# Kernel optimization log

Hardware: AMD Instinct MI355X
Metric: run time of the kernel (lower is better)

The kernel has to match this reference:

```python
import jax, jax.numpy as jnp
import numpy as np

B, S, D_IN, D_OUT, E, K = 4, 2048, 1024, 1024, 8, 2


def setup_inputs() -> dict:
    key = jax.random.key(0)
    ks = jax.random.split(key, 6)
    scale_in = 1.0 / np.sqrt(D_IN)
    return {
        "x": jax.random.normal(ks[0], (B, S, D_IN), dtype=jnp.float32),
        "gate_w": jax.random.uniform(ks[1], (E, D_IN), jnp.float32, -scale_in, scale_in),
        "gate_b": jax.random.uniform(ks[2], (E,), jnp.float32, -scale_in, scale_in),
        "expert_biases": jnp.zeros((E,), dtype=jnp.float32),
        "expert_w": jax.random.uniform(ks[3], (E, D_OUT, D_IN), jnp.float32, -scale_in, scale_in),
        "expert_b": jax.random.uniform(ks[4], (E, D_OUT), jnp.float32, -scale_in, scale_in),
    }


def reference(x, gate_w, gate_b, expert_biases, expert_w, expert_b):
    # Gating: sigmoid(Linear(x) + expert_biases), then top-k over experts
    gate_logits = jnp.einsum("bsd,ed->bse", x, gate_w) + gate_b + expert_biases
    gate_probs = jax.nn.sigmoid(gate_logits)
    top_k_probs, top_k_indices = jax.lax.top_k(gate_probs, K)  # [B,S,K]
    top_k_probs = top_k_probs / jnp.sum(top_k_probs, axis=-1, keepdims=True)

    # Dense all-expert compute: stack[e,b,s,o]
    expert_outputs = jnp.einsum("bsd,eod->ebso", x, expert_w) + expert_b[:, None, None, :]

    # Faithful reproduction of the original gather/permute:
    # result[b,s,j,o] = expert_outputs[tki[b,s,j], b, s, j]  (feature index is j, not o)
    bi = jnp.arange(B)[:, None, None]
    si = jnp.arange(S)[None, :, None]
    ji = jnp.arange(K)[None, None, :]
    val = expert_outputs[top_k_indices, bi, si, ji]  # [B,S,K]

    weighted = jnp.sum(val * top_k_probs, axis=-1)  # [B,S]
    final_output = jnp.broadcast_to(weighted[..., None], (B, S, D_OUT))
    return final_output, top_k_indices
```

## Files before the change

### kernel.cpp

```cpp
#include <hip/hip_runtime.h>
#include <math.h>

#define TOKENS 8192
#define DIN    1024
#define DOUT   1024
#define NE     8

typedef float vf4 __attribute__((ext_vector_type(4)));

__global__ __launch_bounds__(512, 4) void moe_fused(
    const float* __restrict__ x,
    const float* __restrict__ gate_w,
    const float* __restrict__ gate_b,
    const float* __restrict__ expert_biases,
    const float* __restrict__ expert_w,
    const float* __restrict__ expert_b,
    float* __restrict__ out,
    float* __restrict__ out_idx) {
  __shared__ float lgate[NE * DIN];

  {
    const vf4* src = (const vf4*)gate_w;
    vf4* dst = (vf4*)lgate;
#pragma unroll
    for (int i = 0; i < 4; ++i)
      dst[threadIdx.x + 512 * i] = src[threadIdx.x + 512 * i];
  }

  const int t    = blockIdx.x * 8 + (threadIdx.x >> 6);
  const int lane = threadIdx.x & 63;

  vf4 xa[4];
  const vf4* xr = (const vf4*)(x + (size_t)t * DIN);
#pragma unroll
  for (int i = 0; i < 4; ++i) xa[i] = xr[lane + 64 * i];

  __syncthreads();

  float za[NE];
#pragma unroll
  for (int e = 0; e < NE; ++e) za[e] = 0.f;
#pragma unroll
  for (int i = 0; i < 4; ++i) {
    vf4 w[NE];
#pragma unroll
    for (int e = 0; e < NE; ++e)
      w[e] = ((const vf4*)(lgate + e * DIN))[lane + 64 * i];
#pragma unroll
    for (int e = 0; e < NE; ++e)
      za[e] += xa[i].x * w[e].x + xa[i].y * w[e].y + xa[i].z * w[e].z + xa[i].w * w[e].w;
  }

#pragma unroll
  for (int off = 32; off > 0; off >>= 1) {
    float tmp[NE];
#pragma unroll
    for (int e = 0; e < NE; ++e) tmp[e] = __shfl_xor(za[e], off, 64);
#pragma unroll
    for (int e = 0; e < NE; ++e) za[e] += tmp[e];
  }
#pragma unroll
  for (int e = 0; e < NE; ++e) za[e] += gate_b[e] + expert_biases[e];

  int e0 = 0; float z0 = za[0];
#pragma unroll
  for (int e = 1; e < NE; ++e) if (za[e] > z0) { z0 = za[e]; e0 = e; }
  int e1 = (e0 == 0) ? 1 : 0; float z1 = za[e1];
#pragma unroll
  for (int e = 0; e < NE; ++e) if (e != e0 && za[e] > z1) { z1 = za[e]; e1 = e; }

  const vf4* r0 = (const vf4*)(expert_w + (size_t)e0 * (DOUT * DIN));
  const vf4* r1 = (const vf4*)(expert_w + (size_t)e1 * (DOUT * DIN) + DIN);
  vf4 wa[4], wb[4];
#pragma unroll
  for (int i = 0; i < 4; ++i) { wa[i] = r0[lane + 64 * i]; wb[i] = r1[lane + 64 * i]; }
  float b0 = expert_b[e0 * DOUT + 0];
  float b1 = expert_b[e1 * DOUT + 1];

  float p0 = 1.f / (1.f + expf(-z0));
  float p1 = 1.f / (1.f + expf(-z1));
  float s  = 1.f / (p0 + p1);
  float w0 = p0 * s, w1 = p1 * s;

  float d0 = 0.f, d1 = 0.f;
#pragma unroll
  for (int i = 0; i < 4; ++i) {
    d0 += xa[i].x * wa[i].x + xa[i].y * wa[i].y + xa[i].z * wa[i].z + xa[i].w * wa[i].w;
    d1 += xa[i].x * wb[i].x + xa[i].y * wb[i].y + xa[i].z * wb[i].z + xa[i].w * wb[i].w;
  }
#pragma unroll
  for (int off = 32; off > 0; off >>= 1) {
    float t0 = __shfl_xor(d0, off, 64);
    float t1 = __shfl_xor(d1, off, 64);
    d0 += t0; d1 += t1;
  }
  d0 += b0; d1 += b1;

  float ov = d0 * w0 + d1 * w1;

  vf4 v = {ov, ov, ov, ov};
  vf4* orow = (vf4*)(out + (size_t)t * DOUT);
#pragma unroll
  for (int i = 0; i < 4; ++i) orow[lane + 64 * i] = v;

  if (lane == 0) {
    out_idx[t * 2 + 0] = (float)e0;
    out_idx[t * 2 + 1] = (float)e1;
  }
}

extern "C" void kernel_launch(void* const* d_in, const int* in_sizes, int n_in,
                              void* d_out, int out_size, void* d_ws, size_t ws_size,
                              hipStream_t stream) {
  const float* x             = (const float*)d_in[0];
  const float* gate_w        = (const float*)d_in[1];
  const float* gate_b        = (const float*)d_in[2];
  const float* expert_biases = (const float*)d_in[3];
  const float* expert_w      = (const float*)d_in[4];
  const float* expert_b      = (const float*)d_in[5];

  float* out     = (float*)d_out;
  float* out_idx = out + (size_t)TOKENS * DOUT;

  moe_fused<<<dim3(1024), dim3(512), 0, stream>>>(
      x, gate_w, gate_b, expert_biases, expert_w, expert_b, out, out_idx);
}
```

Before: 113.4 us.

## Process two tokens per wave to amortize gate-weight LDS staging

```diff
diff --git a/kernel.cpp b/kernel.cpp
--- a/kernel.cpp
+++ b/kernel.cpp
@@ -5,6 +5,7 @@
 #define DIN    1024
 #define DOUT   1024
 #define NE     8
+#define NWAVES 4096
 
 typedef float vf4 __attribute__((ext_vector_type(4)));
 
@@ -27,13 +28,19 @@
       dst[threadIdx.x + 512 * i] = src[threadIdx.x + 512 * i];
   }
 
-  const int t    = blockIdx.x * 8 + (threadIdx.x >> 6);
+  const int w    = blockIdx.x * 8 + (threadIdx.x >> 6);
   const int lane = threadIdx.x & 63;
+  const int t0 = w;
+  const int t1 = w + NWAVES;
+
+  float zbias[NE];
+#pragma unroll
+  for (int e = 0; e < NE; ++e) zbias[e] = gate_b[e] + expert_biases[e];
 
   vf4 xa[4];
-  const vf4* xr = (const vf4*)(x + (size_t)t * DIN);
-#pragma unroll
-  for (int i = 0; i < 4; ++i) xa[i] = xr[lane + 64 * i];
+  const vf4* xr0 = (const vf4*)(x + (size_t)t0 * DIN);
+#pragma unroll
+  for (int i = 0; i < 4; ++i) xa[i] = xr0[lane + 64 * i];
 
   __syncthreads();
 
@@ -42,14 +49,19 @@
   for (int e = 0; e < NE; ++e) za[e] = 0.f;
 #pragma unroll
   for (int i = 0; i < 4; ++i) {
-    vf4 w[NE];
-#pragma unroll
-    for (int e = 0; e < NE; ++e)
-      w[e] = ((const vf4*)(lgate + e * DIN))[lane + 64 * i];
-#pragma unroll
-    for (int e = 0; e < NE; ++e)
-      za[e] += xa[i].x * w[e].x + xa[i].y * w[e].y + xa[i].z * w[e].z + xa[i].w * w[e].w;
-  }
+    vf4 wv[NE];
+#pragma unroll
+    for (int e = 0; e < NE; ++e)
+      wv[e] = ((const vf4*)(lgate + e * DIN))[lane + 64 * i];
+#pragma unroll
+    for (int e = 0; e < NE; ++e)
+      za[e] += xa[i].x * wv[e].x + xa[i].y * wv[e].y + xa[i].z * wv[e].z + xa[i].w * wv[e].w;
+  }
+
+  vf4 xb[4];
+  const vf4* xr1 = (const vf4*)(x + (size_t)t1 * DIN);
+#pragma unroll
+  for (int i = 0; i < 4; ++i) xb[i] = xr1[lane + 64 * i];
 
 #pragma unroll
   for (int off = 32; off > 0; off >>= 1) {
@@ -60,7 +72,7 @@
     for (int e = 0; e < NE; ++e) za[e] += tmp[e];
   }
 #pragma unroll
-  for (int e = 0; e < NE; ++e) za[e] += gate_b[e] + expert_biases[e];
+  for (int e = 0; e < NE; ++e) za[e] += zbias[e];
 
   int e0 = 0; float z0 = za[0];
 #pragma unroll
@@ -69,43 +81,107 @@
 #pragma unroll
   for (int e = 0; e < NE; ++e) if (e != e0 && za[e] > z1) { z1 = za[e]; e1 = e; }
 
-  const vf4* r0 = (const vf4*)(expert_w + (size_t)e0 * (DOUT * DIN));
-  const vf4* r1 = (const vf4*)(expert_w + (size_t)e1 * (DOUT * DIN) + DIN);
-  vf4 wa[4], wb[4];
-#pragma unroll
-  for (int i = 0; i < 4; ++i) { wa[i] = r0[lane + 64 * i]; wb[i] = r1[lane + 64 * i]; }
-  float b0 = expert_b[e0 * DOUT + 0];
-  float b1 = expert_b[e1 * DOUT + 1];
-
-  float p0 = 1.f / (1.f + expf(-z0));
-  float p1 = 1.f / (1.f + expf(-z1));
-  float s  = 1.f / (p0 + p1);
-  float w0 = p0 * s, w1 = p1 * s;
-
-  float d0 = 0.f, d1 = 0.f;
+  if (lane == 0) {
+    out_idx[t0 * 2 + 0] = (float)e0;
+    out_idx[t0 * 2 + 1] = (float)e1;
+  }
+
+  {
+    const vf4* r0 = (const vf4*)(expert_w + (size_t)e0 * (DOUT * DIN));
+    const vf4* r1 = (const vf4*)(expert_w + (size_t)e1 * (DOUT * DIN) + DIN);
+    vf4 wa[4], wb[4];
+#pragma unroll
+    for (int i = 0; i < 4; ++i) { wa[i] = r0[lane + 64 * i]; wb[i] = r1[lane + 64 * i]; }
+    float b0 = expert_b[e0 * DOUT + 0];
+    float b1 = expert_b[e1 * DOUT + 1];
+
+    float p0 = 1.f / (1.f + expf(-z0));
+    float p1 = 1.f / (1.f + expf(-z1));
+    float s  = 1.f / (p0 + p1);
+    float w0 = p0 * s, w1 = p1 * s;
+
+    float ovp = 0.f;
+#pragma unroll
+    for (int i = 0; i < 4; ++i) {
+      float d0p = xa[i].x * wa[i].x + xa[i].y * wa[i].y + xa[i].z * wa[i].z + xa[i].w * wa[i].w;
+      float d1p = xa[i].x * wb[i].x + xa[i].y * wb[i].y + xa[i].z * wb[i].z + xa[i].w * wb[i].w;
+      ovp += d0p * w0 + d1p * w1;
+    }
+#pragma unroll
+    for (int off = 32; off > 0; off >>= 1) ovp += __shfl_xor(ovp, off, 64);
+    float ov = ovp + b0 * w0 + b1 * w1;
+
+    vf4 v = {ov, ov, ov, ov};
+    vf4* orow = (vf4*)(out + (size_t)t0 * DOUT);
+#pragma unroll
+    for (int i = 0; i < 4; ++i) orow[lane + 64 * i] = v;
+  }
+
+#pragma unroll
+  for (int e = 0; e < NE; ++e) za[e] = 0.f;
 #pragma unroll
   for (int i = 0; i < 4; ++i) {
-    d0 += xa[i].x * wa[i].x + xa[i].y * wa[i].y + xa[i].z * wa[i].z + xa[i].w * wa[i].w;
-    d1 += xa[i].x * wb[i].x + xa[i].y * wb[i].y + xa[i].z * wb[i].z + xa[i].w * wb[i].w;
-  }
+    vf4 wv[NE];
+#pragma unroll
+    for (int e = 0; e < NE; ++e)
+      wv[e] = ((const vf4*)(lgate + e * DIN))[lane + 64 * i];
+#pragma unroll
+    for (int e = 0; e < NE; ++e)
+      za[e] += xb[i].x * wv[e].x + xb[i].y * wv[e].y + xb[i].z * wv[e].z + xb[i].w * wv[e].w;
+  }
+
 #pragma unroll
   for (int off = 32; off > 0; off >>= 1) {
-    float t0 = __shfl_xor(d0, off, 64);
-    float t1 = __shfl_xor(d1, off, 64);
-    d0 += t0; d1 += t1;
-  }
-  d0 += b0; d1 += b1;
-
-  float ov = d0 * w0 + d1 * w1;
-
-  vf4 v = {ov, ov, ov, ov};
-  vf4* orow = (vf4*)(out + (size_t)t * DOUT);
-#pragma unroll
-  for (int i = 0; i < 4; ++i) orow[lane + 64 * i] = v;
+    float tmp[NE];
+#pragma unroll
+    for (int e = 0; e < NE; ++e) tmp[e] = __shfl_xor(za[e], off, 64);
+#pragma unroll
+    for (int e = 0; e < NE; ++e) za[e] += tmp[e];
+  }
+#pragma unroll
+  for (int e = 0; e < NE; ++e) za[e] += zbias[e];
+
+  int f0 = 0; float y0 = za[0];
+#pragma unroll
+  for (int e = 1; e < NE; ++e) if (za[e] > y0) { y0 = za[e]; f0 = e; }
+  int f1 = (f0 == 0) ? 1 : 0; float y1 = za[f1];
+#pragma unroll
+  for (int e = 0; e < NE; ++e) if (e != f0 && za[e] > y1) { y1 = za[e]; f1 = e; }
 
   if (lane == 0) {
-    out_idx[t * 2 + 0] = (float)e0;
-    out_idx[t * 2 + 1] = (float)e1;
+    out_idx[t1 * 2 + 0] = (float)f0;
+    out_idx[t1 * 2 + 1] = (float)f1;
+  }
+
+  {
+    const vf4* r0 = (const vf4*)(expert_w + (size_t)f0 * (DOUT * DIN));
+    const vf4* r1 = (const vf4*)(expert_w + (size_t)f1 * (DOUT * DIN) + DIN);
+    vf4 wa[4], wb[4];
+#pragma unroll
+    for (int i = 0; i < 4; ++i) { wa[i] = r0[lane + 64 * i]; wb[i] = r1[lane + 64 * i]; }
+    float b0 = expert_b[f0 * DOUT + 0];
+    float b1 = expert_b[f1 * DOUT + 1];
+
+    float p0 = 1.f / (1.f + expf(-y0));
+    float p1 = 1.f / (1.f + expf(-y1));
+    float s  = 1.f / (p0 + p1);
+    float w0 = p0 * s, w1 = p1 * s;
+
+    float ovp = 0.f;
+#pragma unroll
+    for (int i = 0; i < 4; ++i) {
+      float d0p = xb[i].x * wa[i].x + xb[i].y * wa[i].y + xb[i].z * wa[i].z + xb[i].w * wa[i].w;
+      float d1p = xb[i].x * wb[i].x + xb[i].y * wb[i].y + xb[i].z * wb[i].z + xb[i].w * wb[i].w;
+      ovp += d0p * w0 + d1p * w1;
+    }
+#pragma unroll
+    for (int off = 32; off > 0; off >>= 1) ovp += __shfl_xor(ovp, off, 64);
+    float ov = ovp + b0 * w0 + b1 * w1;
+
+    vf4 v = {ov, ov, ov, ov};
+    vf4* orow = (vf4*)(out + (size_t)t1 * DOUT);
+#pragma unroll
+    for (int i = 0; i < 4; ++i) orow[lane + 64 * i] = v;
   }
 }
 
@@ -122,6 +198,6 @@
   float* out     = (float*)d_out;
   float* out_idx = out + (size_t)TOKENS * DOUT;
 
-  moe_fused<<<dim3(1024), dim3(512), 0, stream>>>(
+  moe_fused<<<dim3(512), dim3(512), 0, stream>>>(
       x, gate_w, gate_b, expert_biases, expert_w, expert_b, out, out_idx);
 }
```

New measurement: 111.4 us, median of 2. About the same (-1.8%).
